# Kernel tuning notes

Measured on AMD Instinct MI355X. Metric: run time of the kernel, lower is better.

Reference implementation:

```python
import jax, jax.numpy as jnp
import numpy as np


def setup_inputs() -> dict:
    key = jax.random.key(0)
    ks = jax.random.split(key, 9)
    B, C, H, W = 16, 512, 64, 64
    s = 1.0 / np.sqrt(C)  # fan-in style init scale for 1x1 conv weights
    x = jax.random.normal(ks[0], (B, C, H, W), dtype=jnp.float32)
    W_theta = jax.random.normal(ks[1], (C, C), dtype=jnp.float32) * s
    b_theta = jax.random.normal(ks[2], (C,), dtype=jnp.float32) * 0.01
    W_phi = jax.random.normal(ks[3], (C, C), dtype=jnp.float32) * s
    b_phi = jax.random.normal(ks[4], (C,), dtype=jnp.float32) * 0.01
    W_g = jax.random.normal(ks[5], (C, C), dtype=jnp.float32) * s
    b_g = jax.random.normal(ks[6], (C,), dtype=jnp.float32) * 0.01
    W_out = jax.random.normal(ks[7], (C, C), dtype=jnp.float32) * s
    b_out = jax.random.normal(ks[8], (C,), dtype=jnp.float32) * 0.01
    return {
        "x": x,
        "W_theta": W_theta, "b_theta": b_theta,
        "W_phi": W_phi, "b_phi": b_phi,
        "W_g": W_g, "b_g": b_g,
        "W_out": W_out, "b_out": b_out,
    }


def reference(x, W_theta, b_theta, W_phi, b_phi, W_g, b_g, W_out, b_out):
    B, C, H, W = x.shape
    n = H * W
    xf = x.reshape(B, C, n)  # [B, C, HW]

    def conv1x1(Wm, b):
        # 1x1 conv == channel-mixing GEMM: [O,C] x [B,C,N] -> [B,O,N]
        return jnp.einsum('oc,bcn->bon', Wm, xf) + b[None, :, None]

    phi = conv1x1(W_phi, b_phi)      # [B, C, HW]
    theta = conv1x1(W_theta, b_theta)  # [B, C, HW] (used transposed: 'b (h w) c')
    g = conv1x1(W_g, b_g)            # [B, C, HW]

    # phi @ theta^T over spatial dim -> [B, C, C] channel-channel attention
    scores = jnp.einsum('bcn,bdn->bcd', phi, theta) * (1.0 / C)
    attn = jax.nn.softmax(scores, axis=2)  # softmax over last (dim=2), as in torch
    Y = jnp.einsum('bcd,bdn->bcn', attn, g)  # [B, C, HW]

    A = jnp.einsum('oc,bcn->bon', W_out, Y) + b_out[None, :, None]
    return x + A.reshape(B, C, H, W)
```

## Files before the change

kernel.cpp:

```cpp
#include <hip/hip_runtime.h>
#include <hip/hip_bf16.h>
#include <stdint.h>


typedef unsigned short u16;
typedef __attribute__((ext_vector_type(8))) short frag8;
typedef __attribute__((ext_vector_type(4))) float f32x4;

__device__ __forceinline__ u16 f2bf(float f) {
  union { __hip_bfloat16 h; u16 u; } c; c.h = __float2bfloat16(f); return c.u;
}

__device__ __forceinline__ void gl_lds16(const u16* g, u16* l) {
  __builtin_amdgcn_global_load_lds(
      (const __attribute__((address_space(1))) void*)g,
      (__attribute__((address_space(3))) void*)l, 16, 0, 0);
}

#define SCHED0 __builtin_amdgcn_sched_barrier(0)
#define SBAR   __builtin_amdgcn_s_barrier()

__global__ __launch_bounds__(256) void prep_x(const float* __restrict__ X,
                                              u16* __restrict__ XT,
                                              u16* __restrict__ XB,
                                              float* __restrict__ S) {
  const int b = blockIdx.z;
  const int n0 = blockIdx.x * 64;
  const int c0 = blockIdx.y * 64;
  __shared__ u16 t[64][72];
  const float* Xb = X + (int64_t)b * (512LL * 4096);
  const int tid = threadIdx.x;
  const int r = tid >> 3;
  const int e8 = (tid & 7) * 8;
#pragma unroll
  for (int p = 0; p < 2; p++) {
    const int row = p * 32 + r;
    const int c = c0 + row;
    const float4 f0 = *(const float4*)(Xb + (int64_t)c * 4096 + n0 + e8);
    const float4 f1 = *(const float4*)(Xb + (int64_t)c * 4096 + n0 + e8 + 4);
    union { uint4 q; u16 u[8]; } pk;
    pk.u[0] = f2bf(f0.x); pk.u[1] = f2bf(f0.y); pk.u[2] = f2bf(f0.z); pk.u[3] = f2bf(f0.w);
    pk.u[4] = f2bf(f1.x); pk.u[5] = f2bf(f1.y); pk.u[6] = f2bf(f1.z); pk.u[7] = f2bf(f1.w);
    *(uint4*)(XB + ((int64_t)b * 512 + c) * 4096 + n0 + e8) = pk.q;
    *(uint4*)&t[row][e8 ^ (row & 56)] = pk.q;
    float s = f0.x + f0.y + f0.z + f0.w + f1.x + f1.y + f1.z + f1.w;
    s += __shfl_xor(s, 1); s += __shfl_xor(s, 2); s += __shfl_xor(s, 4);
    if ((tid & 7) == 0) atomicAdd(&S[b * 512 + c], s);
  }
  __syncthreads();
#pragma unroll
  for (int p = 0; p < 2; p++) {
    const int nr = p * 32 + r;
    union { uint4 q; u16 u[8]; } o;
#pragma unroll
    for (int j = 0; j < 8; j++)
      o.u[j] = t[e8 + j][nr ^ e8];
    *(uint4*)(XT + ((int64_t)b * 4096 + n0 + nr) * 512 + c0 + e8) = o.q;
  }
}

__constant__ const int g_ty[10] = {0,0,0,0,1,1,1,2,2,3};
__constant__ const int g_tx[10] = {0,1,2,3,1,2,3,2,3,3};

__global__ __launch_bounds__(256) void gram_sk(const u16* __restrict__ XB,
                                               float* __restrict__ P) {
  const int z = blockIdx.z;
  const int b = z >> 2, sp = z & 3;
  const int tl = blockIdx.x;
  const int m0 = g_ty[tl] * 128, n0 = g_tx[tl] * 128;
  const int tid = threadIdx.x;
  const int lane = tid & 63, wave = tid >> 6;
  __shared__ u16 sA[3][4096];
  __shared__ u16 sB[3][4096];
  const u16* Xb = XB + (int64_t)b * (512LL * 4096) + sp * 1024;

  f32x4 acc[4][4];
#pragma unroll
  for (int i = 0; i < 4; i++)
#pragma unroll
    for (int j = 0; j < 4; j++)
#pragma unroll
      for (int r = 0; r < 4; r++) acc[i][j][r] = 0.0f;

  const int fr = lane & 15;
  const int fk = (lane >> 4) * 8;
  const int wm = (wave & 1) * 64, wn = (wave >> 1) * 64;

  const int srow = tid >> 2;
  const int scol = (tid & 3) * 8;
  const u16* Ar0 = Xb + (int64_t)(m0 + srow) * 4096 + scol;
  const u16* Ar1 = Xb + (int64_t)(m0 + 64 + srow) * 4096 + scol;
  const u16* Br0 = Xb + (int64_t)(n0 + srow) * 4096 + scol;
  const u16* Br1 = Xb + (int64_t)(n0 + 64 + srow) * 4096 + scol;

  auto stage = [&](int t, int buf) {
    gl_lds16(Ar0 + t * 32, sA[buf] + tid * 8);
    gl_lds16(Ar1 + t * 32, sA[buf] + 2048 + tid * 8);
    gl_lds16(Br0 + t * 32, sB[buf] + tid * 8);
    gl_lds16(Br1 + t * 32, sB[buf] + 2048 + tid * 8);
  };
  auto comp = [&](int buf) {
    frag8 af[4], bf[4];
#pragma unroll
    for (int i = 0; i < 4; i++) {
      af[i] = *(const frag8*)(sA[buf] + (wm + i * 16 + fr) * 32 + fk);
      bf[i] = *(const frag8*)(sB[buf] + (wn + i * 16 + fr) * 32 + fk);
    }
#pragma unroll
    for (int i = 0; i < 4; i++)
#pragma unroll
      for (int j = 0; j < 4; j++)
        acc[i][j] = __builtin_amdgcn_mfma_f32_16x16x32_bf16(af[i], bf[j], acc[i][j], 0, 0, 0);
  };

  stage(0, 0); stage(1, 1);
#pragma unroll
  for (int t = 0; t < 30; t++) {
    SCHED0; SBAR; SCHED0;
    stage(t + 2, (t + 2) % 3);
    asm volatile("s_waitcnt vmcnt(8)" ::: "memory");
    SBAR; SCHED0;
    comp(t % 3);
  }
  asm volatile("s_waitcnt vmcnt(0)" ::: "memory");
  SBAR; SCHED0;
  comp(30 % 3); comp(31 % 3);

  float* Pz = P + (int64_t)z * 262144;
  const int quad = lane >> 4;
#pragma unroll
  for (int i = 0; i < 4; i++)
#pragma unroll
    for (int j = 0; j < 4; j++) {
      const int row0 = m0 + wm + i * 16 + quad * 4;
      const int col = n0 + wn + j * 16 + fr;
#pragma unroll
      for (int r = 0; r < 4; r++)
        Pz[(int64_t)(row0 + r) * 512 + col] = acc[i][j][r];
      if (m0 != n0)
        *(f32x4*)(Pz + (int64_t)col * 512 + row0) = acc[i][j];
    }
}

__global__ __launch_bounds__(256) void reduce_G(const float* __restrict__ P,
                                                u16* __restrict__ G) {
  const int64_t t = (int64_t)blockIdx.x * 256 + threadIdx.x;
  const int b = (int)(t >> 16);
  const int64_t i = (t & 65535) * 4;
  const float* P0 = P + ((int64_t)b * 4) * 262144 + i;
  const float4 a = *(const float4*)(P0);
  const float4 c = *(const float4*)(P0 + 262144);
  const float4 d = *(const float4*)(P0 + 2 * 262144);
  const float4 e = *(const float4*)(P0 + 3 * 262144);
  union { u16 u[4]; uint2 v; } o;
  o.u[0] = f2bf(a.x + c.x + d.x + e.x);
  o.u[1] = f2bf(a.y + c.y + d.y + e.y);
  o.u[2] = f2bf(a.z + c.z + d.z + e.z);
  o.u[3] = f2bf(a.w + c.w + d.w + e.w);
  *(uint2*)(G + (int64_t)b * 262144 + i) = o.v;
}

enum { EPI_BF16 = 0, EPI_SCORES = 1, EPI_BF16I = 2 };

template <int EPI>
__global__ __launch_bounds__(256) void gemm128_bt(
    const u16* __restrict__ A, int64_t sAb, int lda,
    const u16* __restrict__ B, int64_t sBb, int ldb,
    void* __restrict__ Cv, int64_t sCb, int ldc,
    const float* __restrict__ e_bphi, const float* __restrict__ e_btheta,
    const float* __restrict__ e_uphi, const float* __restrict__ e_utheta) {
  const int b = blockIdx.z;
  const int m0 = blockIdx.y * 128, n0 = blockIdx.x * 128;
  const int tid = threadIdx.x;
  const int lane = tid & 63, wave = tid >> 6;
  __shared__ u16 sA[4][4096];
  __shared__ u16 sB[4][4096];
  const u16* Ab = A + (int64_t)b * sAb;
  const u16* Bb = B + (int64_t)b * sBb;

  f32x4 acc[4][4];
#pragma unroll
  for (int i = 0; i < 4; i++)
#pragma unroll
    for (int j = 0; j < 4; j++)
#pragma unroll
      for (int r = 0; r < 4; r++) acc[i][j][r] = 0.0f;

  const int srow = tid >> 2;
  const int scol = (tid & 3) * 8;
  const int fr = lane & 15;
  const int fk = (lane >> 4) * 8;
  const int wm = (wave & 1) * 64, wn = (wave >> 1) * 64;

  const u16* Ar0 = Ab + (int64_t)(m0 + srow) * lda + scol;
  const u16* Ar1 = Ab + (int64_t)(m0 + 64 + srow) * lda + scol;
  const u16* Br0 = Bb + (int64_t)(n0 + srow) * ldb + scol;
  const u16* Br1 = Bb + (int64_t)(n0 + 64 + srow) * ldb + scol;

  auto stage = [&](int t, int buf) {
    gl_lds16(Ar0 + t * 32, sA[buf] + tid * 8);
    gl_lds16(Ar1 + t * 32, sA[buf] + 2048 + tid * 8);
    gl_lds16(Br0 + t * 32, sB[buf] + tid * 8);
    gl_lds16(Br1 + t * 32, sB[buf] + 2048 + tid * 8);
  };
  auto comp = [&](int buf) {
    frag8 af[4], bf[4];
#pragma unroll
    for (int i = 0; i < 4; i++) {
      af[i] = *(const frag8*)(sA[buf] + (wm + i * 16 + fr) * 32 + fk);
      bf[i] = *(const frag8*)(sB[buf] + (wn + i * 16 + fr) * 32 + fk);
    }
#pragma unroll
    for (int i = 0; i < 4; i++)
#pragma unroll
      for (int j = 0; j < 4; j++)
        acc[i][j] = __builtin_amdgcn_mfma_f32_16x16x32_bf16(af[i], bf[j], acc[i][j], 0, 0, 0);
  };

  stage(0, 0); stage(1, 1); stage(2, 2);
#pragma unroll
  for (int t = 0; t < 13; t++) {
    SCHED0; SBAR; SCHED0;
    stage(t + 3, (t + 3) % 4);
    asm volatile("s_waitcnt vmcnt(12)" ::: "memory");
    SBAR; SCHED0;
    comp(t % 4);
  }
  asm volatile("s_waitcnt vmcnt(8)" ::: "memory");
  SBAR; SCHED0;
  comp(13 % 4);
  asm volatile("s_waitcnt vmcnt(4)" ::: "memory");
  SBAR; SCHED0;
  comp(14 % 4);
  asm volatile("s_waitcnt vmcnt(0)" ::: "memory");
  SBAR; SCHED0;
  comp(15 % 4);

  const int quad = lane >> 4;
#pragma unroll
  for (int i = 0; i < 4; i++)
#pragma unroll
    for (int j = 0; j < 4; j++)
#pragma unroll
      for (int r = 0; r < 4; r++) {
        const int row = m0 + wm + i * 16 + quad * 4 + r;
        const int col = n0 + wn + j * 16 + fr;
        const float a = acc[i][j][r];
        if constexpr (EPI == EPI_BF16) {
          ((u16*)Cv)[(int64_t)b * sCb + (int64_t)row * ldc + col] = f2bf(a);
        } else if constexpr (EPI == EPI_BF16I) {
          ((u16*)Cv)[(int64_t)b * sCb + (int64_t)row * ldc + col] =
              f2bf(a + (row == col ? 1.0f : 0.0f));
        } else {
          const float bp = e_bphi[row];
          const float bt = e_btheta[col];
          ((float*)Cv)[(int64_t)b * sCb + (int64_t)row * ldc + col] =
              (a + bp * e_utheta[b * 512 + col] + bt * e_uphi[b * 512 + row] +
               4096.0f * bp * bt) * (1.0f / 512.0f);
        }
      }
}

__global__ __launch_bounds__(256) void gemm_final(const u16* __restrict__ M,
                                                  const u16* __restrict__ XT,
                                                  const float* __restrict__ V,
                                                  float* __restrict__ O) {
  const int b = blockIdx.z;
  const int m0 = blockIdx.y * 128, n0 = blockIdx.x * 128;
  const int tid = threadIdx.x;
  const int lane = tid & 63, wave = tid >> 6;
  __shared__ u16 sA[2][4096];
  __shared__ u16 sB[2][4096];
  const u16* Ab = M + (int64_t)b * 262144;
  const u16* Bb = XT + (int64_t)b * (4096LL * 512);

  f32x4 acc[4][4];
#pragma unroll
  for (int i = 0; i < 4; i++)
#pragma unroll
    for (int j = 0; j < 4; j++)
#pragma unroll
      for (int r = 0; r < 4; r++) acc[i][j][r] = 0.0f;

  const int srow = tid >> 2;
  const int scol = (tid & 3) * 8;
  const int fr = lane & 15;
  const int fk = (lane >> 4) * 8;
  const int wm = (wave & 1) * 64, wn = (wave >> 1) * 64;

  const u16* Ar0 = Ab + (int64_t)(m0 + srow) * 512 + scol;
  const u16* Ar1 = Ab + (int64_t)(m0 + 64 + srow) * 512 + scol;
  const u16* Br0 = Bb + (int64_t)(n0 + srow) * 512 + scol;
  const u16* Br1 = Bb + (int64_t)(n0 + 64 + srow) * 512 + scol;

  gl_lds16(Ar0, sA[0] + tid * 8);
  gl_lds16(Ar1, sA[0] + 2048 + tid * 8);
  gl_lds16(Br0, sB[0] + tid * 8);
  gl_lds16(Br1, sB[0] + 2048 + tid * 8);
  __syncthreads();

  for (int k0 = 0; k0 < 512; k0 += 32) {
    const int cur = (k0 >> 5) & 1;
    if (k0 + 32 < 512) {
      u16* dA = sA[cur ^ 1];
      u16* dB = sB[cur ^ 1];
      gl_lds16(Ar0 + k0 + 32, dA + tid * 8);
      gl_lds16(Ar1 + k0 + 32, dA + 2048 + tid * 8);
      gl_lds16(Br0 + k0 + 32, dB + tid * 8);
      gl_lds16(Br1 + k0 + 32, dB + 2048 + tid * 8);
    }
    frag8 af[4], bf[4];
#pragma unroll
    for (int i = 0; i < 4; i++) {
      af[i] = *(const frag8*)(sA[cur] + (wm + i * 16 + fr) * 32 + fk);
      bf[i] = *(const frag8*)(sB[cur] + (wn + i * 16 + fr) * 32 + fk);
    }
#pragma unroll
    for (int i = 0; i < 4; i++)
#pragma unroll
      for (int j = 0; j < 4; j++)
        acc[i][j] = __builtin_amdgcn_mfma_f32_16x16x32_bf16(af[i], bf[j], acc[i][j], 0, 0, 0);
    __syncthreads();
  }

  const int quad = lane >> 4;
#pragma unroll
  for (int i = 0; i < 4; i++)
#pragma unroll
    for (int j = 0; j < 4; j++)
#pragma unroll
      for (int r = 0; r < 4; r++) {
        const int row = m0 + wm + i * 16 + quad * 4 + r;
        const int col = n0 + wn + j * 16 + fr;
        O[(int64_t)b * (512LL * 4096) + (int64_t)row * 4096 + col] =
            acc[i][j][r] + V[b * 512 + row];
      }
}

__global__ __launch_bounds__(512) void uv_kernel(const float* __restrict__ Wphi,
                                                 const float* __restrict__ Wtheta,
                                                 const float* __restrict__ S,
                                                 float* __restrict__ UPH, float* __restrict__ UTH) {
  const int b = blockIdx.x;
  const int o = threadIdx.x;
  __shared__ float s[512];
  s[o] = S[b * 512 + o];
  __syncthreads();
  float a0 = 0.f, a1 = 0.f;
  for (int c4 = 0; c4 < 512; c4 += 4) {
    const float4 wa = *(const float4*)(Wphi + o * 512 + c4);
    const float4 wb = *(const float4*)(Wtheta + o * 512 + c4);
    a0 += wa.x * s[c4] + wa.y * s[c4 + 1] + wa.z * s[c4 + 2] + wa.w * s[c4 + 3];
    a1 += wb.x * s[c4] + wb.y * s[c4 + 1] + wb.z * s[c4 + 2] + wb.w * s[c4 + 3];
  }
  UPH[b * 512 + o] = a0;
  UTH[b * 512 + o] = a1;
}

__global__ __launch_bounds__(512) void v_kernel(const float* __restrict__ Wout,
                                                const float* __restrict__ R,
                                                const float* __restrict__ bout,
                                                float* __restrict__ V) {
  const int b = blockIdx.x;
  const int o = threadIdx.x;
  __shared__ float s[512];
  s[o] = R[b * 512 + o];
  __syncthreads();
  float a0 = 0.f;
  for (int c4 = 0; c4 < 512; c4 += 4) {
    const float4 wa = *(const float4*)(Wout + o * 512 + c4);
    a0 += wa.x * s[c4] + wa.y * s[c4 + 1] + wa.z * s[c4 + 2] + wa.w * s[c4 + 3];
  }
  V[b * 512 + o] = a0 + bout[o];
}

__global__ __launch_bounds__(256) void convert_w(const float* __restrict__ W0,
                                                 const float* __restrict__ W1,
                                                 const float* __restrict__ W2,
                                                 u16* __restrict__ O0, u16* __restrict__ O1,
                                                 u16* __restrict__ O2) {
  const int idx = blockIdx.x * 256 + threadIdx.x;
  const int m = idx >> 16;
  const int off = (idx & 65535) * 4;
  const float* src = (m == 0) ? W0 : (m == 1) ? W1 : W2;
  u16* dst = (m == 0) ? O0 : (m == 1) ? O1 : O2;
  const float4 f = *(const float4*)(src + off);
  union { u16 u[4]; uint2 v; } p;
  p.u[0] = f2bf(f.x); p.u[1] = f2bf(f.y); p.u[2] = f2bf(f.z); p.u[3] = f2bf(f.w);
  *(uint2*)(dst + off) = p.v;
}

__global__ void wg_transpose(const float* __restrict__ Wg, u16* __restrict__ WgT) {
  __shared__ float t[16][17];
  const int i0 = blockIdx.y * 16, j0 = blockIdx.x * 16;
  t[threadIdx.y][threadIdx.x] = Wg[(i0 + threadIdx.y) * 512 + j0 + threadIdx.x];
  __syncthreads();
  WgT[(j0 + threadIdx.y) * 512 + i0 + threadIdx.x] = f2bf(t[threadIdx.x][threadIdx.y]);
}

__global__ __launch_bounds__(64) void softmax_k(float* __restrict__ SC,
                                                const float* __restrict__ bg,
                                                float* __restrict__ R) {
  const int row = blockIdx.x;
  const int lane = threadIdx.x;
  float* Sr = SC + (int64_t)row * 512;
  union { float4 q[2]; float v[8]; } u;
  u.q[0] = *(const float4*)(Sr + lane * 8);
  u.q[1] = *(const float4*)(Sr + lane * 8 + 4);
  const float4 g0 = *(const float4*)(bg + lane * 8);
  const float4 g1 = *(const float4*)(bg + lane * 8 + 4);
  const float gb[8] = { g0.x, g0.y, g0.z, g0.w, g1.x, g1.y, g1.z, g1.w };
  float m = u.v[0];
#pragma unroll
  for (int j = 1; j < 8; j++) m = fmaxf(m, u.v[j]);
#pragma unroll
  for (int off = 32; off > 0; off >>= 1) m = fmaxf(m, __shfl_xor(m, off));
  float e[8], s = 0.f, sb = 0.f;
#pragma unroll
  for (int j = 0; j < 8; j++) {
    e[j] = __expf(u.v[j] - m);
    s += e[j];
    sb += e[j] * gb[j];
  }
#pragma unroll
  for (int off = 32; off > 0; off >>= 1) { s += __shfl_xor(s, off); sb += __shfl_xor(sb, off); }
  const float inv = 1.0f / s;
  union { uint4 q; u16 h[8]; } o;
#pragma unroll
  for (int j = 0; j < 8; j++) o.h[j] = f2bf(e[j] * inv);
  *(uint4*)((u16*)SC + (int64_t)row * 1024 + lane * 8) = o.q;
  if (lane == 0) R[row] = sb * inv;
}

extern "C" void kernel_launch(void* const* d_in, const int* in_sizes, int n_in,
                              void* d_out, int out_size, void* d_ws, size_t ws_size,
                              hipStream_t stream) {
  const float* x      = (const float*)d_in[0];
  const float* Wtheta = (const float*)d_in[1];
  const float* btheta = (const float*)d_in[2];
  const float* Wphi   = (const float*)d_in[3];
  const float* bphi   = (const float*)d_in[4];
  const float* Wg     = (const float*)d_in[5];
  const float* bg     = (const float*)d_in[6];
  const float* Wout   = (const float*)d_in[7];
  const float* bout   = (const float*)d_in[8];

  char* ws = (char*)d_ws;
  u16*   xT     = (u16*)(ws + 0);
  u16*   G      = (u16*)(ws + 67108864);
  u16*   T1     = (u16*)(ws + 75497472);
  float* SC     = (float*)(ws + 83886080);
  u16*   Wphib  = (u16*)(ws + 100663296);
  u16*   Wthetab= (u16*)(ws + 101187584);
  u16*   Woutb  = (u16*)(ws + 101711872);
  u16*   WgTb   = (u16*)(ws + 102236160);
  float* S      = (float*)(ws + 102760448);
  float* UPH    = (float*)(ws + 102793216);
  float* UTH    = (float*)(ws + 102825984);
  float* R      = (float*)(ws + 102858752);
  float* V      = (float*)(ws + 102891520);
  u16* ATT = (u16*)SC;
  u16* Q = G;
  u16* M = T1;

  u16*   XB = (u16*)d_out;
  float* P  = (float*)((char*)d_out + 67108864);

  hipMemsetAsync(S, 0, 32768, stream);
  prep_x<<<dim3(64, 8, 16), 256, 0, stream>>>(x, xT, XB, S);
  uv_kernel<<<16, 512, 0, stream>>>(Wphi, Wtheta, S, UPH, UTH);
  convert_w<<<768, 256, 0, stream>>>(Wphi, Wtheta, Wout, Wphib, Wthetab, Woutb);
  wg_transpose<<<dim3(32, 32), dim3(16, 16), 0, stream>>>(Wg, WgTb);
  gram_sk<<<dim3(10, 1, 64), 256, 0, stream>>>(XB, P);
  reduce_G<<<4096, 256, 0, stream>>>(P, G);
  gemm128_bt<EPI_BF16><<<dim3(4, 4, 16), 256, 0, stream>>>(
      Wphib, 0, 512, G, 512LL * 512, 512, T1, 512LL * 512, 512,
      nullptr, nullptr, nullptr, nullptr);
  gemm128_bt<EPI_SCORES><<<dim3(4, 4, 16), 256, 0, stream>>>(
      T1, 512LL * 512, 512, Wthetab, 0, 512, SC, 512LL * 512, 512,
      bphi, btheta, UPH, UTH);
  softmax_k<<<8192, 64, 0, stream>>>(SC, bg, R);
  gemm128_bt<EPI_BF16><<<dim3(4, 4, 16), 256, 0, stream>>>(
      WgTb, 0, 512, ATT, 512LL * 1024, 1024, Q, 512LL * 512, 512,
      nullptr, nullptr, nullptr, nullptr);
  gemm128_bt<EPI_BF16I><<<dim3(4, 4, 16), 256, 0, stream>>>(
      Woutb, 0, 512, Q, 512LL * 512, 512, M, 512LL * 512, 512,
      nullptr, nullptr, nullptr, nullptr);
  v_kernel<<<16, 512, 0, stream>>>(Wout, R, bout, V);
  gemm_final<<<dim3(32, 4, 16), 256, 0, stream>>>(M, xT, V, (float*)d_out);
}
```

Baseline: 542.2 us.

## Swizzle LDS tiles in GEMMs and replace atomic row sums with partials

Applies an XOR swizzle to the LDS column layout in the gram and both GEMM kernels, used consistently on the global-to-LDS writes and the MFMA fragment reads, to cut LDS bank conflicts. It also drops the atomicAdd row sums in prep_x and the memset: each block now writes per-block partial sums into the P scratch, and uv_kernel reduces the 64 partials per row. This removes atomic contention and one memset launch, at the cost of extra partial-sum traffic and reusing the P buffer before gram_sk overwrites it.

```diff
diff --git a/kernel.cpp b/kernel.cpp
--- a/kernel.cpp
+++ b/kernel.cpp
@@ -23,7 +23,7 @@
 __global__ __launch_bounds__(256) void prep_x(const float* __restrict__ X,
                                               u16* __restrict__ XT,
                                               u16* __restrict__ XB,
-                                              float* __restrict__ S) {
+                                              float* __restrict__ SP) {
   const int b = blockIdx.z;
   const int n0 = blockIdx.x * 64;
   const int c0 = blockIdx.y * 64;
@@ -45,7 +45,8 @@
     *(uint4*)&t[row][e8 ^ (row & 56)] = pk.q;
     float s = f0.x + f0.y + f0.z + f0.w + f1.x + f1.y + f1.z + f1.w;
     s += __shfl_xor(s, 1); s += __shfl_xor(s, 2); s += __shfl_xor(s, 4);
-    if ((tid & 7) == 0) atomicAdd(&S[b * 512 + c], s);
+    if ((tid & 7) == 0)
+      SP[((int64_t)b * 512 + c) * 64 + blockIdx.x] = s;
   }
   __syncthreads();
 #pragma unroll
@@ -83,11 +84,11 @@
       for (int r = 0; r < 4; r++) acc[i][j][r] = 0.0f;
 
   const int fr = lane & 15;
-  const int fk = (lane >> 4) * 8;
+  const int fkx = (((lane >> 4) ^ ((fr >> 1) & 3))) * 8;
   const int wm = (wave & 1) * 64, wn = (wave >> 1) * 64;
 
   const int srow = tid >> 2;
-  const int scol = (tid & 3) * 8;
+  const int scol = (((tid & 3) ^ ((tid >> 3) & 3))) * 8;
   const u16* Ar0 = Xb + (int64_t)(m0 + srow) * 4096 + scol;
   const u16* Ar1 = Xb + (int64_t)(m0 + 64 + srow) * 4096 + scol;
   const u16* Br0 = Xb + (int64_t)(n0 + srow) * 4096 + scol;
@@ -103,8 +104,8 @@
     frag8 af[4], bf[4];
 #pragma unroll
     for (int i = 0; i < 4; i++) {
-      af[i] = *(const frag8*)(sA[buf] + (wm + i * 16 + fr) * 32 + fk);
-      bf[i] = *(const frag8*)(sB[buf] + (wn + i * 16 + fr) * 32 + fk);
+      af[i] = *(const frag8*)(sA[buf] + (wm + i * 16 + fr) * 32 + fkx);
+      bf[i] = *(const frag8*)(sB[buf] + (wn + i * 16 + fr) * 32 + fkx);
     }
 #pragma unroll
     for (int i = 0; i < 4; i++)
@@ -187,9 +188,9 @@
       for (int r = 0; r < 4; r++) acc[i][j][r] = 0.0f;
 
   const int srow = tid >> 2;
-  const int scol = (tid & 3) * 8;
+  const int scol = (((tid & 3) ^ ((tid >> 3) & 3))) * 8;
   const int fr = lane & 15;
-  const int fk = (lane >> 4) * 8;
+  const int fkx = (((lane >> 4) ^ ((fr >> 1) & 3))) * 8;
   const int wm = (wave & 1) * 64, wn = (wave >> 1) * 64;
 
   const u16* Ar0 = Ab + (int64_t)(m0 + srow) * lda + scol;
@@ -207,8 +208,8 @@
     frag8 af[4], bf[4];
 #pragma unroll
     for (int i = 0; i < 4; i++) {
-      af[i] = *(const frag8*)(sA[buf] + (wm + i * 16 + fr) * 32 + fk);
-      bf[i] = *(const frag8*)(sB[buf] + (wn + i * 16 + fr) * 32 + fk);
+      af[i] = *(const frag8*)(sA[buf] + (wm + i * 16 + fr) * 32 + fkx);
+      bf[i] = *(const frag8*)(sB[buf] + (wn + i * 16 + fr) * 32 + fkx);
     }
 #pragma unroll
     for (int i = 0; i < 4; i++)
@@ -283,9 +284,9 @@
       for (int r = 0; r < 4; r++) acc[i][j][r] = 0.0f;
 
   const int srow = tid >> 2;
-  const int scol = (tid & 3) * 8;
+  const int scol = (((tid & 3) ^ ((tid >> 3) & 3))) * 8;
   const int fr = lane & 15;
-  const int fk = (lane >> 4) * 8;
+  const int fkx = (((lane >> 4) ^ ((fr >> 1) & 3))) * 8;
   const int wm = (wave & 1) * 64, wn = (wave >> 1) * 64;
 
   const u16* Ar0 = Ab + (int64_t)(m0 + srow) * 512 + scol;
@@ -312,8 +313,8 @@
     frag8 af[4], bf[4];
 #pragma unroll
     for (int i = 0; i < 4; i++) {
-      af[i] = *(const frag8*)(sA[cur] + (wm + i * 16 + fr) * 32 + fk);
-      bf[i] = *(const frag8*)(sB[cur] + (wn + i * 16 + fr) * 32 + fk);
+      af[i] = *(const frag8*)(sA[cur] + (wm + i * 16 + fr) * 32 + fkx);
+      bf[i] = *(const frag8*)(sB[cur] + (wn + i * 16 + fr) * 32 + fkx);
     }
 #pragma unroll
     for (int i = 0; i < 4; i++)
@@ -339,12 +340,19 @@
 
 __global__ __launch_bounds__(512) void uv_kernel(const float* __restrict__ Wphi,
                                                  const float* __restrict__ Wtheta,
-                                                 const float* __restrict__ S,
+                                                 const float* __restrict__ SP,
                                                  float* __restrict__ UPH, float* __restrict__ UTH) {
   const int b = blockIdx.x;
   const int o = threadIdx.x;
   __shared__ float s[512];
-  s[o] = S[b * 512 + o];
+  const float* sp = SP + ((int64_t)b * 512 + o) * 64;
+  float a = 0.f;
+#pragma unroll
+  for (int g = 0; g < 64; g += 4) {
+    const float4 q = *(const float4*)(sp + g);
+    a += q.x + q.y + q.z + q.w;
+  }
+  s[o] = a;
   __syncthreads();
   float a0 = 0.f, a1 = 0.f;
   for (int c4 = 0; c4 < 512; c4 += 4) {
@@ -454,7 +462,6 @@
   u16*   Wthetab= (u16*)(ws + 101187584);
   u16*   Woutb  = (u16*)(ws + 101711872);
   u16*   WgTb   = (u16*)(ws + 102236160);
-  float* S      = (float*)(ws + 102760448);
   float* UPH    = (float*)(ws + 102793216);
   float* UTH    = (float*)(ws + 102825984);
   float* R      = (float*)(ws + 102858752);
@@ -465,10 +472,10 @@
 
   u16*   XB = (u16*)d_out;
   float* P  = (float*)((char*)d_out + 67108864);
-
-  hipMemsetAsync(S, 0, 32768, stream);
-  prep_x<<<dim3(64, 8, 16), 256, 0, stream>>>(x, xT, XB, S);
-  uv_kernel<<<16, 512, 0, stream>>>(Wphi, Wtheta, S, UPH, UTH);
+  float* SP = P;
+
+  prep_x<<<dim3(64, 8, 16), 256, 0, stream>>>(x, xT, XB, SP);
+  uv_kernel<<<16, 512, 0, stream>>>(Wphi, Wtheta, SP, UPH, UTH);
   convert_w<<<768, 256, 0, stream>>>(Wphi, Wtheta, Wout, Wphib, Wthetab, Woutb);
   wg_transpose<<<dim3(32, 32), dim3(16, 16), 0, stream>>>(Wg, WgTb);
   gram_sk<<<dim3(10, 1, 64), 256, 0, stream>>>(XB, P);
```

Result: no change. 544.8 us (+0.5%).
